# Performance work log

Hardware: AMD Instinct MI355X
Metric: run time of the kernel (lower is better)

Reference implementation:

```python
import jax, jax.numpy as jnp
import numpy as np

D_MODEL = 256
D_CONV = 4
EXPAND = 2
D_INNER = EXPAND * D_MODEL  # 512


def silu(v):
    return v * jax.nn.sigmoid(v)


def setup_inputs() -> dict:
    key = jax.random.key(0)
    k0, k1, k2, k3, k4 = jax.random.split(key, 5)
    B, H, W = 4, 128, 128
    x = jax.random.normal(k0, (B, H, W, D_MODEL), jnp.float32)
    # nn.Linear(d_model, 2*d_inner, bias=False) -> weight (2*d_inner, d_model)
    W_in = jax.random.normal(k1, (2 * D_INNER, D_MODEL), jnp.float32) * 0.02
    # depthwise nn.Conv1d(d_inner, d_inner, k=4, groups=d_inner) -> weight (d_inner, 1, k)
    conv_w = jax.random.normal(k2, (D_INNER, 1, D_CONV), jnp.float32) * 0.1
    conv_b = jax.random.normal(k3, (D_INNER,), jnp.float32) * 0.02
    # nn.Linear(d_inner, d_model, bias=False) -> weight (d_model, d_inner)
    W_out = jax.random.normal(k4, (D_MODEL, D_INNER), jnp.float32) * 0.02
    return {"x": x, "W_in": W_in, "conv_w": conv_w, "conv_b": conv_b, "W_out": W_out}


def reference(x, W_in, conv_w, conv_b, W_out):
    B, H, W, C = x.shape
    L = H * W
    x_flat = x.reshape(B, L, C)
    xz = jnp.einsum('blc,dc->bld', x_flat, W_in)         # (B, L, 2*d_inner)
    x_branch, z_branch = jnp.split(xz, 2, axis=-1)
    # depthwise conv1d with padding=d_conv-1 then truncate to L == left-pad by d_conv-1
    u = jax.lax.conv_general_dilated(
        x_branch.transpose(0, 2, 1),                      # (B, D, L)
        conv_w,                                           # (D, 1, K)
        window_strides=(1,),
        padding=[(D_CONV - 1, 0)],
        dimension_numbers=('NCH', 'OIH', 'NCH'),
        feature_group_count=D_INNER,
    )
    u = (u + conv_b[None, :, None]).transpose(0, 2, 1)    # (B, L, D)
    u = silu(u)
    # selective_scan in the source is a stub that returns its input unchanged,
    # so the four directional passes reduce to identity transforms of u.
    y1 = u
    y2 = jnp.flip(jnp.flip(u, axis=1), axis=1)
    u_t = u.reshape(B, H, W, -1).transpose(0, 2, 1, 3).reshape(B, L, -1)
    y3 = u_t.reshape(B, W, H, -1).transpose(0, 2, 1, 3).reshape(B, L, -1)
    y4 = jnp.flip(jnp.flip(u_t, axis=1), axis=1).reshape(B, W, H, -1).transpose(0, 2, 1, 3).reshape(B, L, -1)
    y = (y1 + y2 + y3 + y4) * silu(z_branch)
    out = jnp.einsum('bld,cd->blc', y, W_out)
    return out.reshape(B, H, W, C)
```

## Files before the change

kernel.cpp:

```cpp
#include <hip/hip_runtime.h>

#define LSEQ   16384
#define BLROWS 65536
#define DM     256
#define DI     512
#define DXZ    1024

#define BM 128
#define BN 128
#define BK 64

typedef __attribute__((ext_vector_type(8))) short s16x8;
typedef __attribute__((ext_vector_type(4))) short s16x4;
typedef __attribute__((ext_vector_type(4))) float f32x4;

__device__ __forceinline__ float bf2f(unsigned short h) {
  union { unsigned u; float f; } c; c.u = ((unsigned)h) << 16; return c.f;
}
__device__ __forceinline__ unsigned short f2bf(float f) {
  union { float f; unsigned u; } c; c.f = f;
  unsigned u = c.u;
  return (unsigned short)((u + 0x7fffu + ((u >> 16) & 1u)) >> 16);
}

__global__ __launch_bounds__(256)
void cvt_f32_bf16(const float* __restrict__ src, unsigned short* __restrict__ dst, int n4) {
  for (int i = blockIdx.x * blockDim.x + threadIdx.x; i < n4; i += gridDim.x * blockDim.x) {
    const float4 v = reinterpret_cast<const float4*>(src)[i];
    s16x4 o;
    o[0] = (short)f2bf(v.x);
    o[1] = (short)f2bf(v.y);
    o[2] = (short)f2bf(v.z);
    o[3] = (short)f2bf(v.w);
    reinterpret_cast<s16x4*>(dst)[i] = o;
  }
}

__device__ __forceinline__ void gload16(const void* g, void* l) {
  __builtin_amdgcn_global_load_lds((__attribute__((address_space(1))) void*)(g),
                                   (__attribute__((address_space(3))) void*)(l),
                                   16, 0, 0);
}

__device__ __forceinline__ int xswz(int row, int byteInRow) {
  return row * 128 + (byteInRow ^ ((row & 7) << 4));
}

__global__ __launch_bounds__(256, 2)
void gemm1_conv(const unsigned short* __restrict__ A,
                const unsigned short* __restrict__ Bw,
                const float* __restrict__ cw,
                const float* __restrict__ cb,
                unsigned short* __restrict__ Y) {
  __shared__ unsigned short lds[2][BM * BK + BN * BK];

  const int tid  = threadIdx.x;
  const int lane = tid & 63;
  const int wv   = tid >> 6;
  const int wr   = wv >> 1;
  const int wc   = wv & 1;
  const int m0   = blockIdx.y * BM;
  const int n0x  = blockIdx.x * 64;

  const int srow = tid >> 3;
  const int scol = (tid & 7) * 8;

  f32x4 acc[4][4];
#pragma unroll
  for (int i = 0; i < 4; ++i)
#pragma unroll
    for (int j = 0; j < 4; ++j)
#pragma unroll
      for (int r = 0; r < 4; ++r) acc[i][j][r] = 0.f;

  auto stage = [&](int ks, int buf) {
    const unsigned short* Ag = A + (size_t)(m0 + srow) * DM + ks * BK + scol;
    unsigned short* lA = &lds[buf][0]       + tid * 8;
    unsigned short* lB = &lds[buf][BM * BK] + tid * 8;
#pragma unroll
    for (int i = 0; i < 4; ++i) {
      gload16(Ag + (size_t)(i * 32) * DM, lA + i * 2048);
      const int lr   = srow + i * 32;
      const int grow = (i < 2) ? (n0x + lr) : (448 + n0x + lr);
      gload16(Bw + (size_t)grow * DM + ks * BK + scol, lB + i * 2048);
    }
  };

  stage(0, 0);

  const int kSteps = DM / BK;
  for (int ks = 0; ks < kSteps; ++ks) {
    const int cur = ks & 1;
    __syncthreads();
    if (ks + 1 < kSteps) stage(ks + 1, cur ^ 1);

    const unsigned short* lA = &lds[cur][0];
    const unsigned short* lB = &lds[cur][BM * BK];
    const int lrow = lane & 15;
#pragma unroll
    for (int kk = 0; kk < BK; kk += 32) {
      const int lk = kk + ((lane >> 4) << 3);
      s16x8 af[4], bf[4];
#pragma unroll
      for (int i = 0; i < 4; ++i)
        af[i] = *(const s16x8*)(lA + (wr * 64 + i * 16 + lrow) * BK + lk);
#pragma unroll
      for (int j = 0; j < 4; ++j)
        bf[j] = *(const s16x8*)(lB + (wc * 64 + j * 16 + lrow) * BK + lk);
#pragma unroll
      for (int i = 0; i < 4; ++i)
#pragma unroll
        for (int j = 0; j < 4; ++j)
          acc[i][j] = __builtin_amdgcn_mfma_f32_16x16x32_bf16(af[i], bf[j], acc[i][j], 0, 0, 0);
    }
  }

  __syncthreads();
  char* ldsb = (char*)&lds[0][0];
  const int r0 = (lane >> 4) * 4;
  const int c0 = lane & 15;

  if (wc == 0) {
#pragma unroll
    for (int i = 0; i < 4; ++i)
#pragma unroll
      for (int j = 0; j < 4; ++j)
#pragma unroll
        for (int r = 0; r < 4; ++r) {
          const int row = wr * 64 + i * 16 + r0 + r;
          const int col = j * 16 + c0;
          *(unsigned short*)(ldsb + xswz(row + 3, col * 2)) = f2bf(acc[i][j][r]);
        }
  } else {
#pragma unroll
    for (int i = 0; i < 4; ++i)
#pragma unroll
      for (int j = 0; j < 4; ++j)
#pragma unroll
        for (int r = 0; r < 4; ++r) {
          const int row = wr * 64 + i * 16 + r0 + r;
          const int col = j * 16 + c0;
          *(unsigned short*)(ldsb + 16768 + xswz(row, col * 2)) = f2bf(acc[i][j][r]);
        }
  }

  if (tid < 192) {
    const int hi = tid >> 6;
    const int hc = tid & 63;
    float s = 0.f;
    if ((m0 & (LSEQ - 1)) != 0) {
      const unsigned short* xr = A  + (size_t)(m0 - 3 + hi) * DM;
      const unsigned short* wr_ = Bw + (size_t)(n0x + hc) * DM;
#pragma unroll
      for (int kk = 0; kk < DM; kk += 8) {
        const s16x8 xa = *(const s16x8*)(xr + kk);
        const s16x8 wa = *(const s16x8*)(wr_ + kk);
#pragma unroll
        for (int j = 0; j < 8; ++j)
          s += bf2f((unsigned short)xa[j]) * bf2f((unsigned short)wa[j]);
      }
    }
    *(unsigned short*)(ldsb + xswz(hi, hc * 2)) = f2bf(s);
  }
  __syncthreads();

  const int rr2 = tid >> 1;
  const int cb2 = (tid & 1) * 32;
#pragma unroll
  for (int v = 0; v < 4; ++v) {
    const int c = cb2 + v * 8;
    const s16x8 t0 = *(const s16x8*)(ldsb + xswz(rr2 + 0, c * 2));
    const s16x8 t1 = *(const s16x8*)(ldsb + xswz(rr2 + 1, c * 2));
    const s16x8 t2 = *(const s16x8*)(ldsb + xswz(rr2 + 2, c * 2));
    const s16x8 t3 = *(const s16x8*)(ldsb + xswz(rr2 + 3, c * 2));
    const s16x8 zv = *(const s16x8*)(ldsb + 16768 + xswz(rr2, c * 2));
    s16x8 o;
#pragma unroll
    for (int j = 0; j < 8; ++j) {
      const int ch = n0x + c + j;
      const float4 w4 = *(const float4*)(cw + (size_t)ch * 4);
      float a = cb[ch];
      a += w4.x * bf2f((unsigned short)t0[j]);
      a += w4.y * bf2f((unsigned short)t1[j]);
      a += w4.z * bf2f((unsigned short)t2[j]);
      a += w4.w * bf2f((unsigned short)t3[j]);
      const float su = a * __builtin_amdgcn_rcpf(1.f + __expf(-a));
      const float z  = bf2f((unsigned short)zv[j]);
      const float sz = z * __builtin_amdgcn_rcpf(1.f + __expf(-z));
      o[j] = (short)f2bf(4.f * su * sz);
    }
    *(s16x8*)(Y + (size_t)(m0 + rr2) * DI + n0x + c) = o;
  }
}

__global__ __launch_bounds__(256, 2)
void gemm_bt_f32(const unsigned short* __restrict__ A,
                 const unsigned short* __restrict__ B,
                 float* __restrict__ C,
                 int M, int N, int K) {
  __shared__ unsigned short lds[2][BM * BK + BN * BK];

  const int tid  = threadIdx.x;
  const int lane = tid & 63;
  const int wv   = tid >> 6;
  const int wr   = wv >> 1;
  const int wc   = wv & 1;
  const int m0   = blockIdx.y * BM;
  const int n0   = blockIdx.x * BN;

  const int srow = tid >> 3;
  const int scol = (tid & 7) * 8;

  const int kSteps = K / BK;

  f32x4 acc[4][4];
#pragma unroll
  for (int i = 0; i < 4; ++i)
#pragma unroll
    for (int j = 0; j < 4; ++j)
#pragma unroll
      for (int r = 0; r < 4; ++r) acc[i][j][r] = 0.f;

  auto stage = [&](int ks, int buf) {
    const unsigned short* Ag = A + (size_t)(m0 + srow) * K + ks * BK + scol;
    const unsigned short* Bg = B + (size_t)(n0 + srow) * K + ks * BK + scol;
    unsigned short* lA = &lds[buf][0]       + tid * 8;
    unsigned short* lB = &lds[buf][BM * BK] + tid * 8;
#pragma unroll
    for (int i = 0; i < 4; ++i) {
      gload16(Ag + (size_t)(i * 32) * K, lA + i * 2048);
      gload16(Bg + (size_t)(i * 32) * K, lB + i * 2048);
    }
  };

  stage(0, 0);

  for (int ks = 0; ks < kSteps; ++ks) {
    const int cur = ks & 1;
    __syncthreads();
    if (ks + 1 < kSteps) stage(ks + 1, cur ^ 1);

    const unsigned short* lA = &lds[cur][0];
    const unsigned short* lB = &lds[cur][BM * BK];
    const int lrow = lane & 15;
#pragma unroll
    for (int kk = 0; kk < BK; kk += 32) {
      const int lk = kk + ((lane >> 4) << 3);
      s16x8 af[4], bf[4];
#pragma unroll
      for (int i = 0; i < 4; ++i)
        af[i] = *(const s16x8*)(lA + (wr * 64 + i * 16 + lrow) * BK + lk);
#pragma unroll
      for (int j = 0; j < 4; ++j)
        bf[j] = *(const s16x8*)(lB + (wc * 64 + j * 16 + lrow) * BK + lk);
#pragma unroll
      for (int i = 0; i < 4; ++i)
#pragma unroll
        for (int j = 0; j < 4; ++j)
          acc[i][j] = __builtin_amdgcn_mfma_f32_16x16x32_bf16(af[i], bf[j], acc[i][j], 0, 0, 0);
    }
  }

  const int r0 = (lane >> 4) * 4;
  const int c0 = lane & 15;
#pragma unroll
  for (int i = 0; i < 4; ++i)
#pragma unroll
    for (int j = 0; j < 4; ++j) {
      const int rr = m0 + wr * 64 + i * 16 + r0;
      const int cc = n0 + wc * 64 + j * 16 + c0;
#pragma unroll
      for (int r = 0; r < 4; ++r)
        C[(size_t)(rr + r) * N + cc] = acc[i][j][r];
    }
}

extern "C" void kernel_launch(void* const* d_in, const int* in_sizes, int n_in,
                              void* d_out, int out_size, void* d_ws, size_t ws_size,
                              hipStream_t stream) {
  const float* x      = (const float*)d_in[0];
  const float* W_in   = (const float*)d_in[1];
  const float* conv_w = (const float*)d_in[2];
  const float* conv_b = (const float*)d_in[3];
  const float* W_out  = (const float*)d_in[4];

  char* ws = (char*)d_ws;
  unsigned short* y_bf    = (unsigned short*)(ws);
  unsigned short* x_bf    = (unsigned short*)(ws + (64ull << 20));
  unsigned short* win_bf  = (unsigned short*)(ws + (100ull << 20));
  unsigned short* wout_bf = (unsigned short*)(ws + (101ull << 20));

  cvt_f32_bf16<<<2048, 256, 0, stream>>>(x,     x_bf,    (BLROWS * DM) / 4);
  cvt_f32_bf16<<<256,  256, 0, stream>>>(W_in,  win_bf,  (DXZ * DM) / 4);
  cvt_f32_bf16<<<128,  256, 0, stream>>>(W_out, wout_bf, (DM * DI) / 4);

  gemm1_conv<<<dim3(DI / 64, BLROWS / BM), 256, 0, stream>>>(
      x_bf, win_bf, conv_w, conv_b, y_bf);

  gemm_bt_f32<<<dim3(DM / BN, BLROWS / BM), 256, 0, stream>>>(
      y_bf, wout_bf, (float*)d_out, BLROWS, DM, DI);
}
```

Before: 307.0 us.

## Keep conv epilogue in registers using wave shuffles instead of LDS staging

Each wave now computes matching x and z column tiles, so the depthwise conv and SiLU gating run directly on MFMA accumulators. Cross-row conv history comes from lane shuffles, plus a small LDS patch for tile boundaries. This removes the bf16 round-trip of the whole accumulator tile through LDS and one barrier. The trade-off is scalar 2-byte global stores per element instead of 16-byte vector stores, which may hurt write coalescing. The conv input also stays in fp32 rather than being rounded to bf16.

Measured after the change: 268.3 us. 12.6% less time.

```diff
diff --git a/kernel.cpp b/kernel.cpp
--- a/kernel.cpp
+++ b/kernel.cpp
@@ -42,10 +42,6 @@
                                    16, 0, 0);
 }
 
-__device__ __forceinline__ int xswz(int row, int byteInRow) {
-  return row * 128 + (byteInRow ^ ((row & 7) << 4));
-}
-
 __global__ __launch_bounds__(256, 2)
 void gemm1_conv(const unsigned short* __restrict__ A,
                 const unsigned short* __restrict__ Bw,
@@ -53,25 +49,28 @@
                 const float* __restrict__ cb,
                 unsigned short* __restrict__ Y) {
   __shared__ unsigned short lds[2][BM * BK + BN * BK];
+  __shared__ float patch[2][3][64];
 
   const int tid  = threadIdx.x;
   const int lane = tid & 63;
-  const int wv   = tid >> 6;
-  const int wr   = wv >> 1;
-  const int wc   = wv & 1;
+  const int w    = tid >> 6;
+  const int wr2  = w >> 1;
+  const int wcol = w & 1;
+  const int g    = lane >> 4;
+  const int c0   = lane & 15;
   const int m0   = blockIdx.y * BM;
   const int n0x  = blockIdx.x * 64;
 
   const int srow = tid >> 3;
   const int scol = (tid & 7) * 8;
 
-  f32x4 acc[4][4];
+  f32x4 ax[4][2], az[4][2];
 #pragma unroll
   for (int i = 0; i < 4; ++i)
 #pragma unroll
-    for (int j = 0; j < 4; ++j)
-#pragma unroll
-      for (int r = 0; r < 4; ++r) acc[i][j][r] = 0.f;
+    for (int j = 0; j < 2; ++j)
+#pragma unroll
+      for (int r = 0; r < 4; ++r) { ax[i][j][r] = 0.f; az[i][j][r] = 0.f; }
 
   auto stage = [&](int ks, int buf) {
     const unsigned short* Ag = A + (size_t)(m0 + srow) * DM + ks * BK + scol;
@@ -100,96 +99,87 @@
 #pragma unroll
     for (int kk = 0; kk < BK; kk += 32) {
       const int lk = kk + ((lane >> 4) << 3);
-      s16x8 af[4], bf[4];
-#pragma unroll
-      for (int i = 0; i < 4; ++i)
-        af[i] = *(const s16x8*)(lA + (wr * 64 + i * 16 + lrow) * BK + lk);
-#pragma unroll
-      for (int j = 0; j < 4; ++j)
-        bf[j] = *(const s16x8*)(lB + (wc * 64 + j * 16 + lrow) * BK + lk);
-#pragma unroll
-      for (int i = 0; i < 4; ++i)
-#pragma unroll
-        for (int j = 0; j < 4; ++j)
-          acc[i][j] = __builtin_amdgcn_mfma_f32_16x16x32_bf16(af[i], bf[j], acc[i][j], 0, 0, 0);
-    }
-  }
-
-  __syncthreads();
-  char* ldsb = (char*)&lds[0][0];
-  const int r0 = (lane >> 4) * 4;
-  const int c0 = lane & 15;
-
-  if (wc == 0) {
-#pragma unroll
-    for (int i = 0; i < 4; ++i)
-#pragma unroll
-      for (int j = 0; j < 4; ++j)
-#pragma unroll
-        for (int r = 0; r < 4; ++r) {
-          const int row = wr * 64 + i * 16 + r0 + r;
-          const int col = j * 16 + c0;
-          *(unsigned short*)(ldsb + xswz(row + 3, col * 2)) = f2bf(acc[i][j][r]);
+      s16x8 af[4], bx[2], bz[2];
+#pragma unroll
+      for (int i = 0; i < 4; ++i)
+        af[i] = *(const s16x8*)(lA + (wr2 * 64 + i * 16 + lrow) * BK + lk);
+#pragma unroll
+      for (int j = 0; j < 2; ++j) {
+        bx[j] = *(const s16x8*)(lB + (wcol * 32 + j * 16 + lrow) * BK + lk);
+        bz[j] = *(const s16x8*)(lB + (64 + wcol * 32 + j * 16 + lrow) * BK + lk);
+      }
+#pragma unroll
+      for (int i = 0; i < 4; ++i)
+#pragma unroll
+        for (int j = 0; j < 2; ++j) {
+          ax[i][j] = __builtin_amdgcn_mfma_f32_16x16x32_bf16(af[i], bx[j], ax[i][j], 0, 0, 0);
+          az[i][j] = __builtin_amdgcn_mfma_f32_16x16x32_bf16(af[i], bz[j], az[i][j], 0, 0, 0);
         }
-  } else {
-#pragma unroll
-    for (int i = 0; i < 4; ++i)
-#pragma unroll
-      for (int j = 0; j < 4; ++j)
-#pragma unroll
-        for (int r = 0; r < 4; ++r) {
-          const int row = wr * 64 + i * 16 + r0 + r;
-          const int col = j * 16 + c0;
-          *(unsigned short*)(ldsb + 16768 + xswz(row, col * 2)) = f2bf(acc[i][j][r]);
-        }
-  }
-
+    }
+  }
+
+  if (wr2 == 0 && g == 3) {
+#pragma unroll
+    for (int j = 0; j < 2; ++j) {
+      const int chl = wcol * 32 + j * 16 + c0;
+      patch[1][0][chl] = ax[3][j][1];
+      patch[1][1][chl] = ax[3][j][2];
+      patch[1][2][chl] = ax[3][j][3];
+    }
+  }
   if (tid < 192) {
     const int hi = tid >> 6;
     const int hc = tid & 63;
     float s = 0.f;
     if ((m0 & (LSEQ - 1)) != 0) {
-      const unsigned short* xr = A  + (size_t)(m0 - 3 + hi) * DM;
+      const unsigned short* xr  = A  + (size_t)(m0 - 3 + hi) * DM;
       const unsigned short* wr_ = Bw + (size_t)(n0x + hc) * DM;
 #pragma unroll
       for (int kk = 0; kk < DM; kk += 8) {
         const s16x8 xa = *(const s16x8*)(xr + kk);
         const s16x8 wa = *(const s16x8*)(wr_ + kk);
 #pragma unroll
-        for (int j = 0; j < 8; ++j)
-          s += bf2f((unsigned short)xa[j]) * bf2f((unsigned short)wa[j]);
-      }
-    }
-    *(unsigned short*)(ldsb + xswz(hi, hc * 2)) = f2bf(s);
+        for (int jj = 0; jj < 8; ++jj)
+          s += bf2f((unsigned short)xa[jj]) * bf2f((unsigned short)wa[jj]);
+      }
+    }
+    patch[0][hi][hc] = s;
   }
   __syncthreads();
 
-  const int rr2 = tid >> 1;
-  const int cb2 = (tid & 1) * 32;
-#pragma unroll
-  for (int v = 0; v < 4; ++v) {
-    const int c = cb2 + v * 8;
-    const s16x8 t0 = *(const s16x8*)(ldsb + xswz(rr2 + 0, c * 2));
-    const s16x8 t1 = *(const s16x8*)(ldsb + xswz(rr2 + 1, c * 2));
-    const s16x8 t2 = *(const s16x8*)(ldsb + xswz(rr2 + 2, c * 2));
-    const s16x8 t3 = *(const s16x8*)(ldsb + xswz(rr2 + 3, c * 2));
-    const s16x8 zv = *(const s16x8*)(ldsb + 16768 + xswz(rr2, c * 2));
-    s16x8 o;
-#pragma unroll
-    for (int j = 0; j < 8; ++j) {
-      const int ch = n0x + c + j;
-      const float4 w4 = *(const float4*)(cw + (size_t)ch * 4);
-      float a = cb[ch];
-      a += w4.x * bf2f((unsigned short)t0[j]);
-      a += w4.y * bf2f((unsigned short)t1[j]);
-      a += w4.z * bf2f((unsigned short)t2[j]);
-      a += w4.w * bf2f((unsigned short)t3[j]);
-      const float su = a * __builtin_amdgcn_rcpf(1.f + __expf(-a));
-      const float z  = bf2f((unsigned short)zv[j]);
-      const float sz = z * __builtin_amdgcn_rcpf(1.f + __expf(-z));
-      o[j] = (short)f2bf(4.f * su * sz);
-    }
-    *(s16x8*)(Y + (size_t)(m0 + rr2) * DI + n0x + c) = o;
+  const int src = (lane - 16) & 63;
+#pragma unroll
+  for (int j = 0; j < 2; ++j) {
+    const int chl = wcol * 32 + j * 16 + c0;
+    const int ch  = n0x + chl;
+    const float4 w4 = *(const float4*)(cw + (size_t)ch * 4);
+    const float cbv = cb[ch];
+#pragma unroll
+    for (int i = 0; i < 4; ++i) {
+      const f32x4 curf = ax[i][j];
+      const f32x4 prvf = (i > 0) ? ax[(i > 0 ? i - 1 : 0)][j] : ax[0][j];
+      const float s1 = (g == 3) ? prvf[1] : curf[1];
+      const float s2 = (g == 3) ? prvf[2] : curf[2];
+      const float s3 = (g == 3) ? prvf[3] : curf[3];
+      float vm3 = __shfl(s1, src);
+      float vm2 = __shfl(s2, src);
+      float vm1 = __shfl(s3, src);
+      if (i == 0 && g == 0) {
+        vm3 = patch[wr2][0][chl];
+        vm2 = patch[wr2][1][chl];
+        vm1 = patch[wr2][2][chl];
+      }
+      const float vv[7] = {vm3, vm2, vm1, curf[0], curf[1], curf[2], curf[3]};
+      const int mbase = m0 + wr2 * 64 + i * 16 + g * 4;
+#pragma unroll
+      for (int r = 0; r < 4; ++r) {
+        float a = cbv + w4.x * vv[r] + w4.y * vv[r + 1] + w4.z * vv[r + 2] + w4.w * vv[r + 3];
+        const float su = a * __builtin_amdgcn_rcpf(1.f + __expf(-a));
+        const float z  = az[i][j][r];
+        const float sz = z * __builtin_amdgcn_rcpf(1.f + __expf(-z));
+        Y[(size_t)(mbase + r) * DI + ch] = f2bf(4.f * su * sz);
+      }
+    }
   }
 }
 
```
